# Performance work log

Measured on AMD Instinct MI355X. Metric: run time of the kernel, lower is better.

The kernel has to match this reference:

```python
import jax, jax.numpy as jnp
import numpy as np

B = 16384       # num graphs
N = 524288      # num atoms/nodes
E = 1048576     # num edges
D_EMB = 128     # dim_emb (atom embedding dim from mol_encoder)
D_STATE = 64    # dim_state
D_EDGE = 32     # raw edge_attr feature dim
N_STATES = 10   # dim_state_encoding (embedding vocab)


def setup_inputs() -> dict:
    key = jax.random.key(0)
    ks = jax.random.split(key, 11)
    return {
        "edge_attr": jax.random.normal(ks[0], (E, D_EDGE), dtype=jnp.float32),
        "z_mol": jax.random.normal(ks[1], (B, D_EMB), dtype=jnp.float32),
        "z_atom": jax.random.normal(ks[2], (N, D_EMB), dtype=jnp.float32),
        "state_emb": jax.random.normal(ks[3], (N_STATES, D_STATE), dtype=jnp.float32),
        "W1": jax.random.normal(ks[4], (D_EMB + D_STATE, 32), dtype=jnp.float32) * 0.07,
        "b1": jnp.zeros((32,), dtype=jnp.float32),
        "W2": jax.random.normal(ks[5], (32, 1), dtype=jnp.float32) * 0.18,
        "b2": jnp.zeros((1,), dtype=jnp.float32),
        "state": jax.random.randint(ks[6], (B,), 0, N_STATES),
        "edge_index0": jax.random.randint(ks[7], (E,), 0, N),
        "batch": jnp.sort(jax.random.randint(ks[8], (N,), 0, B)),
    }


def reference(edge_attr, z_mol, z_atom, state_emb, W1, b1, W2, b2,
              state, edge_index0, batch):
    # z_state = self.state_encoder(state)                     [B, Ds]
    z_state = state_emb[state]
    # gather per-node state embedding                         [N, Ds]
    z_state_nodes = z_state[batch]
    # edge_attr = cat([edge_attr, z_state[batch[edge_index[0]]]], 1)  [E, De+Ds]
    edge_attr_out = jnp.concatenate([edge_attr, z_state_nodes[edge_index0]], axis=1)
    # attn = fc_attn(cat([z_atom, z_state[batch]], 1))         [N, 1]
    h = jnp.concatenate([z_atom, z_state_nodes], axis=1)
    logits = jax.nn.leaky_relu(h @ W1 + b1, negative_slope=0.01) @ W2 + b2
    # segment softmax over graphs (PyG torch_geometric.utils.softmax)
    seg_max = jax.ops.segment_max(logits, batch, num_segments=B)   # [B, 1]
    ex = jnp.exp(logits - seg_max[batch])
    seg_sum = jax.ops.segment_sum(ex, batch, num_segments=B)       # [B, 1]
    attn = ex / (seg_sum[batch] + 1e-16)
    # z_mol_state = global_add_pool(attn * z_atom, batch)      [B, D_emb]
    z_mol_state = jax.ops.segment_sum(attn * z_atom, batch, num_segments=B)
    # input to spect_decoder (opaque downstream)               [B, 2*D_emb]
    x = jnp.concatenate([z_mol, z_mol_state], axis=1)
    return (x, edge_attr_out)
```

## Files before the change

### kernel.cpp

```cpp
#include <hip/hip_runtime.h>
#include <math.h>

#define B_GRAPHS 16384
#define N_NODES  524288
#define E_EDGES  1048576
#define D_EMB    128
#define D_STATE  64
#define HID      32
#define PADK     136
#define WPB      4
#define NWIN     (N_NODES / 32)

typedef __attribute__((ext_vector_type(8))) short short8;
typedef __attribute__((ext_vector_type(4))) float f32x4;

__device__ __forceinline__ unsigned short f2bf(float f) {
    unsigned int u = __builtin_bit_cast(unsigned int, f);
    u += 0x7fffu + ((u >> 16) & 1u);
    return (unsigned short)(u >> 16);
}
__device__ __forceinline__ float bf2f(unsigned short s) {
    unsigned int u = ((unsigned int)s) << 16;
    return __builtin_bit_cast(float, u);
}

__global__ __launch_bounds__(256) void offs_kernel(
    const int* __restrict__ batch, int* __restrict__ offs)
{
    int i = blockIdx.x * 256 + threadIdx.x;
    if (i >= N_NODES) return;
    int b = batch[i];
    int prev = (i == 0) ? -1 : batch[i - 1];
    for (int x = prev + 1; x <= b; ++x) offs[x] = i;
    if (i == N_NODES - 1)
        for (int x = b + 1; x <= B_GRAPHS; ++x) offs[x] = N_NODES;
}

__global__ __launch_bounds__(256) void hb_kernel(
    const float* __restrict__ state_emb, const float* __restrict__ W1,
    const float* __restrict__ b1, const int* __restrict__ state,
    float* __restrict__ hb)
{
    int t = threadIdx.x;
    int j = t & 31;
    int g = blockIdx.x * 8 + (t >> 5);
    int st = state[g];
    const float* zs = state_emb + st * D_STATE;
    float acc = b1[j];
    #pragma unroll 8
    for (int k = 0; k < D_STATE; ++k)
        acc += zs[k] * W1[(D_EMB + k) * HID + j];
    hb[g * HID + j] = acc;
}

__global__ __launch_bounds__(256, 3) void window_kernel(
    const float* __restrict__ z_atom,
    const float* __restrict__ W1,
    const float* __restrict__ W2,
    const float* __restrict__ b2,
    const int*   __restrict__ batch,
    const float* __restrict__ hb,
    float*       __restrict__ out_x,
    float*       __restrict__ Sbuf,
    float*       __restrict__ rec_u,
    float*       __restrict__ rec_s,
    int*         __restrict__ rec_id)
{
    __shared__ unsigned short s_w1t[HID][PADK];
    __shared__ unsigned short s_zb[WPB][32][PADK];

    const int t    = threadIdx.x;
    const int lane = t & 63;
    const int w    = t >> 6;
    const int l15  = lane & 15;
    const int kc   = lane >> 4;

    for (int i = t; i < D_EMB * HID; i += 256) {
        int k = i >> 5, j = i & 31;
        s_w1t[j][k] = f2bf(W1[i]);
    }
    __syncthreads();

    const float b2v = b2[0];
    float w2v[2][4];
    #pragma unroll
    for (int jh = 0; jh < 2; ++jh)
        #pragma unroll
        for (int r = 0; r < 4; ++r)
            w2v[jh][r] = W2[16 * jh + 4 * kc + r];

    unsigned short (*zb)[PADK] = s_zb[w];

    const int win = blockIdx.x * WPB + w;
    const int c0  = win * 32;
    int bv = 0;
    if (lane < 32) bv = batch[c0 + lane];

    const int leftN  = (c0 > 0) ? batch[c0 - 1] : -2;
    const int rightN = (c0 + 32 < N_NODES) ? batch[c0 + 32] : -2;

    float4 hbf[2][2];
    #pragma unroll
    for (int nh = 0; nh < 2; ++nh) {
        int bn = __shfl(bv, l15 + 16 * nh);
        hbf[nh][0] = *(const float4*)&hb[(size_t)bn * HID + 4 * kc];
        hbf[nh][1] = *(const float4*)&hb[(size_t)bn * HID + 16 + 4 * kc];
    }

    const float4* za4 = (const float4*)z_atom + (size_t)c0 * (D_EMB / 4);
    #pragma unroll
    for (int half = 0; half < 2; ++half) {
        float4 tmp[8];
        #pragma unroll
        for (int it = 0; it < 8; ++it) {
            int idx = (half * 8 + it) * 64 + lane;
            int n = idx >> 5, c = idx & 31;
            tmp[it] = za4[n * (D_EMB / 4) + c];
        }
        #pragma unroll
        for (int it = 0; it < 8; ++it) {
            int idx = (half * 8 + it) * 64 + lane;
            int n = idx >> 5, c = idx & 31;
            float4 v = tmp[it];
            unsigned lo = (unsigned)f2bf(v.x) | ((unsigned)f2bf(v.y) << 16);
            unsigned hi = (unsigned)f2bf(v.z) | ((unsigned)f2bf(v.w) << 16);
            *(uint2*)&zb[n][c * 4] = make_uint2(lo, hi);
        }
    }

    f32x4 acc[2][2] = {{{0.f,0.f,0.f,0.f},{0.f,0.f,0.f,0.f}},
                       {{0.f,0.f,0.f,0.f},{0.f,0.f,0.f,0.f}}};
    #pragma unroll
    for (int kb = 0; kb < 4; ++kb) {
        short8 a0 = *(const short8*)&s_w1t[l15][kb * 32 + kc * 8];
        short8 a1 = *(const short8*)&s_w1t[16 + l15][kb * 32 + kc * 8];
        short8 q0 = *(const short8*)&zb[l15][kb * 32 + kc * 8];
        short8 q1 = *(const short8*)&zb[16 + l15][kb * 32 + kc * 8];
        acc[0][0] = __builtin_amdgcn_mfma_f32_16x16x32_bf16(a0, q0, acc[0][0], 0, 0, 0);
        acc[1][0] = __builtin_amdgcn_mfma_f32_16x16x32_bf16(a1, q0, acc[1][0], 0, 0, 0);
        acc[0][1] = __builtin_amdgcn_mfma_f32_16x16x32_bf16(a0, q1, acc[0][1], 0, 0, 0);
        acc[1][1] = __builtin_amdgcn_mfma_f32_16x16x32_bf16(a1, q1, acc[1][1], 0, 0, 0);
    }

    float pt[2];
    #pragma unroll
    for (int nh = 0; nh < 2; ++nh) {
        float part = 0.f;
        #pragma unroll
        for (int r = 0; r < 4; ++r) {
            float h = acc[0][nh][r] + (&hbf[nh][0].x)[r];
            h = h > 0.f ? h : 0.01f * h;
            part += h * w2v[0][r];
        }
        #pragma unroll
        for (int r = 0; r < 4; ++r) {
            float h = acc[1][nh][r] + (&hbf[nh][1].x)[r];
            h = h > 0.f ? h : 0.01f * h;
            part += h * w2v[1][r];
        }
        part += __shfl_xor(part, 16);
        part += __shfl_xor(part, 32);
        pt[nh] = __expf(part + b2v);
    }

    float u0 = 0.f, u1 = 0.f, ss = 0.f;
    int cur = __shfl(bv, 0);
    int a = 0;
    bool usedL = false, usedR = false;

    #pragma unroll 4
    for (int n = 0; n < 32; ++n) {
        int bn = __shfl(bv, n);
        if (bn != cur) {
            if (a == 0 && leftN == cur) {
                *(float2*)&rec_u[(size_t)(2 * win) * 128 + lane * 2] = make_float2(u0, u1);
                if (lane == 0) { rec_s[2 * win] = ss; rec_id[2 * win] = cur; }
                usedL = true;
            } else {
                *(float2*)&out_x[(size_t)cur * 256 + 128 + lane * 2] = make_float2(u0, u1);
                if (lane == 0) Sbuf[cur] = ss;
            }
            u0 = u1 = ss = 0.f;
            cur = bn; a = n;
        }
        float pn = (n < 16) ? __shfl(pt[0], n) : __shfl(pt[1], n - 16);
        unsigned zz = *(const unsigned*)&zb[n][lane * 2];
        u0 += pn * bf2f((unsigned short)(zz & 0xffffu));
        u1 += pn * bf2f((unsigned short)(zz >> 16));
        ss += pn;
    }
    {
        bool lb = (a == 0) && (leftN == cur);
        bool rb = (rightN == cur);
        if (lb) {
            *(float2*)&rec_u[(size_t)(2 * win) * 128 + lane * 2] = make_float2(u0, u1);
            if (lane == 0) { rec_s[2 * win] = ss; rec_id[2 * win] = cur; }
            usedL = true;
        } else if (rb) {
            *(float2*)&rec_u[(size_t)(2 * win + 1) * 128 + lane * 2] = make_float2(u0, u1);
            if (lane == 0) { rec_s[2 * win + 1] = ss; rec_id[2 * win + 1] = cur; }
            usedR = true;
        } else {
            *(float2*)&out_x[(size_t)cur * 256 + 128 + lane * 2] = make_float2(u0, u1);
            if (lane == 0) Sbuf[cur] = ss;
        }
    }
    if (lane == 0) {
        if (!usedL) rec_id[2 * win] = -1;
        if (!usedR) rec_id[2 * win + 1] = -1;
    }
}

__global__ __launch_bounds__(256) void combine_kernel(
    const float* __restrict__ z_mol,
    const int*   __restrict__ offs,
    const float* __restrict__ Sbuf,
    const float* __restrict__ rec_u,
    const float* __restrict__ rec_s,
    const int*   __restrict__ rec_id,
    float*       __restrict__ out_x)
{
    const int t = threadIdx.x, lane = t & 63, wv = t >> 6;
    const int g = blockIdx.x * 4 + wv;
    const int gs = offs[g], ge = offs[g + 1];

    float2 U = make_float2(0.f, 0.f);
    float  S = 0.f;
    if (ge > gs) {
        int w0 = gs >> 5, w1 = (ge - 1) >> 5;
        if (w0 == w1) {
            U = *(const float2*)&out_x[(size_t)g * 256 + 128 + lane * 2];
            S = Sbuf[g];
        } else {
            for (int wn = w0; wn <= w1; ++wn) {
                #pragma unroll
                for (int sl = 0; sl < 2; ++sl) {
                    int id = rec_id[2 * wn + sl];
                    if (id == g) {
                        float2 r = *(const float2*)&rec_u[(size_t)(2 * wn + sl) * 128 + lane * 2];
                        U.x += r.x; U.y += r.y;
                        S += rec_s[2 * wn + sl];
                    }
                }
            }
        }
    }
    const float inv = 1.f / (S + 1e-16f);
    float2 zm = *(const float2*)&z_mol[(size_t)g * D_EMB + lane * 2];
    *(float2*)&out_x[(size_t)g * 256 + lane * 2] = zm;
    *(float2*)&out_x[(size_t)g * 256 + 128 + lane * 2] = make_float2(U.x * inv, U.y * inv);
}

__global__ __launch_bounds__(256) void edge_copy_kernel(
    const f32x4* __restrict__ edge_attr4,
    f32x4*       __restrict__ out4)
{
    int tid = blockIdx.x * 256 + threadIdx.x;
    int e = tid >> 3, q = tid & 7;
    f32x4 v = __builtin_nontemporal_load(&edge_attr4[tid]);
    __builtin_nontemporal_store(v, &out4[(size_t)e * 24 + q]);
}

__global__ __launch_bounds__(256) void edge_state_kernel(
    const f32x4* __restrict__ state_emb4,
    const int*   __restrict__ state,
    const int*   __restrict__ eidx,
    const int*   __restrict__ batch,
    f32x4*       __restrict__ out4)
{
    int tid = blockIdx.x * 256 + threadIdx.x;
    int e = tid >> 4, q = tid & 15;
    int n = eidx[e];
    int b = batch[n];
    int s = state[b];
    f32x4 v = state_emb4[s * 16 + q];
    __builtin_nontemporal_store(v, &out4[(size_t)e * 24 + 8 + q]);
}

extern "C" void kernel_launch(void* const* d_in, const int* in_sizes, int n_in,
                              void* d_out, int out_size, void* d_ws, size_t ws_size,
                              hipStream_t stream)
{
    const float* edge_attr = (const float*)d_in[0];
    const float* z_mol     = (const float*)d_in[1];
    const float* z_atom    = (const float*)d_in[2];
    const float* state_emb = (const float*)d_in[3];
    const float* W1        = (const float*)d_in[4];
    const float* b1        = (const float*)d_in[5];
    const float* W2        = (const float*)d_in[6];
    const float* b2        = (const float*)d_in[7];
    const int*   state     = (const int*)d_in[8];
    const int*   eidx      = (const int*)d_in[9];
    const int*   batch     = (const int*)d_in[10];

    float* out_x = (float*)d_out;
    float* out_e = out_x + (size_t)B_GRAPHS * 256;

    int*   offs = (int*)d_ws;
    float* hbuf = (float*)((char*)d_ws + 65552);
    float* Sbuf = (float*)((char*)d_ws + 65552 + (size_t)B_GRAPHS * HID * 4);

    float* recbase = out_e + 80000000ull;
    float* rec_u  = recbase;
    float* rec_s  = rec_u + (size_t)NWIN * 2 * 128;
    int*   rec_id = (int*)(rec_s + (size_t)NWIN * 2);

    offs_kernel<<<N_NODES / 256, 256, 0, stream>>>(batch, offs);
    hb_kernel<<<B_GRAPHS / 8, 256, 0, stream>>>(state_emb, W1, b1, state, hbuf);

    window_kernel<<<NWIN / WPB, 256, 0, stream>>>(
        z_atom, W1, W2, b2, batch, hbuf, out_x, Sbuf, rec_u, rec_s, rec_id);

    combine_kernel<<<B_GRAPHS / 4, 256, 0, stream>>>(
        z_mol, offs, Sbuf, rec_u, rec_s, rec_id, out_x);

    edge_copy_kernel<<<(E_EDGES * 8) / 256, 256, 0, stream>>>(
        (const f32x4*)edge_attr, (f32x4*)out_e);
    edge_state_kernel<<<(E_EDGES * 16) / 256, 256, 0, stream>>>(
        (const f32x4*)state_emb, state, eidx, batch, (f32x4*)out_e);
}
```

Before: 187.6 us.

## Merge prep and edge kernels, keep W1 in registers, raise occupancy

Merges the offsets and hidden-bias kernels into one launch, and the edge-copy and edge-state kernels into another, which removes two launches and the gaps between them. In the window kernel, the bf16 W1 fragments are loaded straight from global memory into registers instead of through a shared-memory transpose. This removes a __syncthreads and frees LDS, and launch_bounds is raised to 4 blocks per SM. z_atom loads become nontemporal. The trade-off is more register pressure and redundant per-wave global reads of W1.

```diff
diff --git a/kernel.cpp b/kernel.cpp
--- a/kernel.cpp
+++ b/kernel.cpp
@@ -24,36 +24,34 @@
     return __builtin_bit_cast(float, u);
 }
 
-__global__ __launch_bounds__(256) void offs_kernel(
-    const int* __restrict__ batch, int* __restrict__ offs)
-{
-    int i = blockIdx.x * 256 + threadIdx.x;
-    if (i >= N_NODES) return;
-    int b = batch[i];
-    int prev = (i == 0) ? -1 : batch[i - 1];
-    for (int x = prev + 1; x <= b; ++x) offs[x] = i;
-    if (i == N_NODES - 1)
-        for (int x = b + 1; x <= B_GRAPHS; ++x) offs[x] = N_NODES;
-}
-
-__global__ __launch_bounds__(256) void hb_kernel(
+__global__ __launch_bounds__(256) void prep_kernel(
+    const int*   __restrict__ batch,
     const float* __restrict__ state_emb, const float* __restrict__ W1,
     const float* __restrict__ b1, const int* __restrict__ state,
-    float* __restrict__ hb)
-{
-    int t = threadIdx.x;
-    int j = t & 31;
-    int g = blockIdx.x * 8 + (t >> 5);
-    int st = state[g];
-    const float* zs = state_emb + st * D_STATE;
-    float acc = b1[j];
-    #pragma unroll 8
-    for (int k = 0; k < D_STATE; ++k)
-        acc += zs[k] * W1[(D_EMB + k) * HID + j];
-    hb[g * HID + j] = acc;
-}
-
-__global__ __launch_bounds__(256, 3) void window_kernel(
+    int* __restrict__ offs, float* __restrict__ hb)
+{
+    const int bid = blockIdx.x, t = threadIdx.x;
+    if (bid < 2048) {
+        int i = bid * 256 + t;
+        int b = batch[i];
+        int prev = (i == 0) ? -1 : batch[i - 1];
+        for (int x = prev + 1; x <= b; ++x) offs[x] = i;
+        if (i == N_NODES - 1)
+            for (int x = b + 1; x <= B_GRAPHS; ++x) offs[x] = N_NODES;
+    } else {
+        int j = t & 31;
+        int g = (bid - 2048) * 8 + (t >> 5);
+        int st = state[g];
+        const float* zs = state_emb + st * D_STATE;
+        float acc = b1[j];
+        #pragma unroll 8
+        for (int k = 0; k < D_STATE; ++k)
+            acc += zs[k] * W1[(D_EMB + k) * HID + j];
+        hb[g * HID + j] = acc;
+    }
+}
+
+__global__ __launch_bounds__(256, 4) void window_kernel(
     const float* __restrict__ z_atom,
     const float* __restrict__ W1,
     const float* __restrict__ W2,
@@ -66,7 +64,6 @@
     float*       __restrict__ rec_s,
     int*         __restrict__ rec_id)
 {
-    __shared__ unsigned short s_w1t[HID][PADK];
     __shared__ unsigned short s_zb[WPB][32][PADK];
 
     const int t    = threadIdx.x;
@@ -75,11 +72,16 @@
     const int l15  = lane & 15;
     const int kc   = lane >> 4;
 
-    for (int i = t; i < D_EMB * HID; i += 256) {
-        int k = i >> 5, j = i & 31;
-        s_w1t[j][k] = f2bf(W1[i]);
-    }
-    __syncthreads();
+    short8 wa[2][4];
+    #pragma unroll
+    for (int jh = 0; jh < 2; ++jh)
+        #pragma unroll
+        for (int kb = 0; kb < 4; ++kb)
+            #pragma unroll
+            for (int i = 0; i < 8; ++i) {
+                int k = kb * 32 + kc * 8 + i;
+                wa[jh][kb][i] = (short)f2bf(W1[k * HID + jh * 16 + l15]);
+            }
 
     const float b2v = b2[0];
     float w2v[2][4];
@@ -107,23 +109,23 @@
         hbf[nh][1] = *(const float4*)&hb[(size_t)bn * HID + 16 + 4 * kc];
     }
 
-    const float4* za4 = (const float4*)z_atom + (size_t)c0 * (D_EMB / 4);
+    const f32x4* za4 = (const f32x4*)z_atom + (size_t)c0 * (D_EMB / 4);
     #pragma unroll
     for (int half = 0; half < 2; ++half) {
-        float4 tmp[8];
+        f32x4 tmp[8];
         #pragma unroll
         for (int it = 0; it < 8; ++it) {
             int idx = (half * 8 + it) * 64 + lane;
             int n = idx >> 5, c = idx & 31;
-            tmp[it] = za4[n * (D_EMB / 4) + c];
+            tmp[it] = __builtin_nontemporal_load(&za4[n * (D_EMB / 4) + c]);
         }
         #pragma unroll
         for (int it = 0; it < 8; ++it) {
             int idx = (half * 8 + it) * 64 + lane;
             int n = idx >> 5, c = idx & 31;
-            float4 v = tmp[it];
-            unsigned lo = (unsigned)f2bf(v.x) | ((unsigned)f2bf(v.y) << 16);
-            unsigned hi = (unsigned)f2bf(v.z) | ((unsigned)f2bf(v.w) << 16);
+            f32x4 v = tmp[it];
+            unsigned lo = (unsigned)f2bf(v[0]) | ((unsigned)f2bf(v[1]) << 16);
+            unsigned hi = (unsigned)f2bf(v[2]) | ((unsigned)f2bf(v[3]) << 16);
             *(uint2*)&zb[n][c * 4] = make_uint2(lo, hi);
         }
     }
@@ -132,14 +134,12 @@
                        {{0.f,0.f,0.f,0.f},{0.f,0.f,0.f,0.f}}};
     #pragma unroll
     for (int kb = 0; kb < 4; ++kb) {
-        short8 a0 = *(const short8*)&s_w1t[l15][kb * 32 + kc * 8];
-        short8 a1 = *(const short8*)&s_w1t[16 + l15][kb * 32 + kc * 8];
         short8 q0 = *(const short8*)&zb[l15][kb * 32 + kc * 8];
         short8 q1 = *(const short8*)&zb[16 + l15][kb * 32 + kc * 8];
-        acc[0][0] = __builtin_amdgcn_mfma_f32_16x16x32_bf16(a0, q0, acc[0][0], 0, 0, 0);
-        acc[1][0] = __builtin_amdgcn_mfma_f32_16x16x32_bf16(a1, q0, acc[1][0], 0, 0, 0);
-        acc[0][1] = __builtin_amdgcn_mfma_f32_16x16x32_bf16(a0, q1, acc[0][1], 0, 0, 0);
-        acc[1][1] = __builtin_amdgcn_mfma_f32_16x16x32_bf16(a1, q1, acc[1][1], 0, 0, 0);
+        acc[0][0] = __builtin_amdgcn_mfma_f32_16x16x32_bf16(wa[0][kb], q0, acc[0][0], 0, 0, 0);
+        acc[1][0] = __builtin_amdgcn_mfma_f32_16x16x32_bf16(wa[1][kb], q0, acc[1][0], 0, 0, 0);
+        acc[0][1] = __builtin_amdgcn_mfma_f32_16x16x32_bf16(wa[0][kb], q1, acc[0][1], 0, 0, 0);
+        acc[1][1] = __builtin_amdgcn_mfma_f32_16x16x32_bf16(wa[1][kb], q1, acc[1][1], 0, 0, 0);
     }
 
     float pt[2];
@@ -251,30 +251,30 @@
     *(float2*)&out_x[(size_t)g * 256 + 128 + lane * 2] = make_float2(U.x * inv, U.y * inv);
 }
 
-__global__ __launch_bounds__(256) void edge_copy_kernel(
+#define NB_COPY (E_EDGES * 8 / 256)
+__global__ __launch_bounds__(256) void edge_kernel(
     const f32x4* __restrict__ edge_attr4,
-    f32x4*       __restrict__ out4)
-{
-    int tid = blockIdx.x * 256 + threadIdx.x;
-    int e = tid >> 3, q = tid & 7;
-    f32x4 v = __builtin_nontemporal_load(&edge_attr4[tid]);
-    __builtin_nontemporal_store(v, &out4[(size_t)e * 24 + q]);
-}
-
-__global__ __launch_bounds__(256) void edge_state_kernel(
     const f32x4* __restrict__ state_emb4,
     const int*   __restrict__ state,
     const int*   __restrict__ eidx,
     const int*   __restrict__ batch,
     f32x4*       __restrict__ out4)
 {
-    int tid = blockIdx.x * 256 + threadIdx.x;
-    int e = tid >> 4, q = tid & 15;
-    int n = eidx[e];
-    int b = batch[n];
-    int s = state[b];
-    f32x4 v = state_emb4[s * 16 + q];
-    __builtin_nontemporal_store(v, &out4[(size_t)e * 24 + 8 + q]);
+    const int bid = blockIdx.x, t = threadIdx.x;
+    if (bid < NB_COPY) {
+        int tid = bid * 256 + t;
+        int e = tid >> 3, q = tid & 7;
+        f32x4 v = __builtin_nontemporal_load(&edge_attr4[tid]);
+        __builtin_nontemporal_store(v, &out4[(size_t)e * 24 + q]);
+    } else {
+        int tid = (bid - NB_COPY) * 256 + t;
+        int e = tid >> 4, q = tid & 15;
+        int n = eidx[e];
+        int b = batch[n];
+        int s = state[b];
+        f32x4 v = state_emb4[s * 16 + q];
+        __builtin_nontemporal_store(v, &out4[(size_t)e * 24 + 8 + q]);
+    }
 }
 
 extern "C" void kernel_launch(void* const* d_in, const int* in_sizes, int n_in,
@@ -305,8 +305,7 @@
     float* rec_s  = rec_u + (size_t)NWIN * 2 * 128;
     int*   rec_id = (int*)(rec_s + (size_t)NWIN * 2);
 
-    offs_kernel<<<N_NODES / 256, 256, 0, stream>>>(batch, offs);
-    hb_kernel<<<B_GRAPHS / 8, 256, 0, stream>>>(state_emb, W1, b1, state, hbuf);
+    prep_kernel<<<4096, 256, 0, stream>>>(batch, state_emb, W1, b1, state, offs, hbuf);
 
     window_kernel<<<NWIN / WPB, 256, 0, stream>>>(
         z_atom, W1, W2, b2, batch, hbuf, out_x, Sbuf, rec_u, rec_s, rec_id);
@@ -314,8 +313,7 @@
     combine_kernel<<<B_GRAPHS / 4, 256, 0, stream>>>(
         z_mol, offs, Sbuf, rec_u, rec_s, rec_id, out_x);
 
-    edge_copy_kernel<<<(E_EDGES * 8) / 256, 256, 0, stream>>>(
-        (const f32x4*)edge_attr, (f32x4*)out_e);
-    edge_state_kernel<<<(E_EDGES * 16) / 256, 256, 0, stream>>>(
-        (const f32x4*)state_emb, state, eidx, batch, (f32x4*)out_e);
-}
+    edge_kernel<<<NB_COPY + (E_EDGES * 16 / 256), 256, 0, stream>>>(
+        (const f32x4*)edge_attr, (const f32x4*)state_emb,
+        state, eidx, batch, (f32x4*)out_e);
+}
```

Result: faster. 171.5 us (-8.5%).
